# Optimization experiments

Hardware: AMD Instinct MI355X
Metric: run time of the kernel (lower is better)

## Reference

```python
import jax, jax.numpy as jnp
import numpy as np

B, C, L = 8, 256, 2048


def setup_inputs() -> dict:
    key = jax.random.key(0)
    ks = jax.random.split(key, 7)
    s = 0.05
    return {
        "x": jax.random.normal(ks[0], (B, C, L), dtype=jnp.float32),
        "Wq": jax.random.normal(ks[1], (C, C), dtype=jnp.float32) * s,
        "bq": jax.random.normal(ks[2], (C,), dtype=jnp.float32) * s,
        "Wk": jax.random.normal(ks[3], (C, C), dtype=jnp.float32) * s,
        "bk": jax.random.normal(ks[4], (C,), dtype=jnp.float32) * s,
        "Wv": jax.random.normal(ks[5], (C, C), dtype=jnp.float32) * s,
        "bv": jax.random.normal(ks[6], (C,), dtype=jnp.float32) * s,
    }


def reference(x, Wq, bq, Wk, bk, Wv, bv):
    # Conv1d with kernel_size=1 == per-position linear over channels.
    # x: [B, C, L]
    scale = x.shape[1] ** (-0.5)
    q = jnp.einsum('oc,bcl->bol', Wq, x) + bq[None, :, None]  # [B,C,L]
    k = jnp.einsum('oc,bcl->bol', Wk, x) + bk[None, :, None]
    v = jnp.einsum('oc,bcl->bol', Wv, x) + bv[None, :, None]
    scores = jnp.einsum('bcl,bcm->blm', q, k) * scale          # [B,L,L]
    attn = jax.nn.softmax(scores, axis=-1)
    context = jnp.einsum('blm,bcm->bcl', attn, v)              # [B,C,L]
    return context + x
```

## Files before the change

### kernel.cpp

```cpp
#include <hip/hip_runtime.h>

#define NB 8
#define NC 256
#define NL 2048
#define SCALE 0.0625f

typedef __attribute__((ext_vector_type(8))) __bf16 bf16x8;
typedef __attribute__((ext_vector_type(4))) float f32x4;
typedef __attribute__((ext_vector_type(4))) unsigned int u32x4;
typedef __attribute__((ext_vector_type(2))) unsigned int u32x2;
typedef __attribute__((ext_vector_type(4))) unsigned short u16x4;
typedef __attribute__((ext_vector_type(8))) unsigned short u16x8;

static __device__ __forceinline__ unsigned short f2b(float f) {
    unsigned int u = __builtin_bit_cast(unsigned int, f);
    u += 0x7fffu + ((u >> 16) & 1u);
    return (unsigned short)(u >> 16);
}

__global__ void wconv_kernel(const float* __restrict__ Wq,
                             const float* __restrict__ Wk,
                             const float* __restrict__ Wv,
                             unsigned short* __restrict__ Wbf)
{
    const int base = (blockIdx.x * 256 + threadIdx.x) * 4;
    const int mat  = base >> 16;
    const int off  = base & 65535;
    const float* W = (mat == 0) ? Wq : (mat == 1) ? Wk : Wv;
    float4 w = *(const float4*)&W[off];
    u16x4 p = {f2b(w.x), f2b(w.y), f2b(w.z), f2b(w.w)};
    *(u16x4*)&Wbf[base] = p;
}

__global__ __launch_bounds__(512, 4) void qkv_mfma(
    const float* __restrict__ x,
    const unsigned short* __restrict__ Wbf,
    const float* __restrict__ bq, const float* __restrict__ bk,
    const float* __restrict__ bv,
    unsigned short* __restrict__ qT, unsigned short* __restrict__ kT,
    unsigned short* __restrict__ vo)
{
    const int raw = blockIdx.x;
    const int b   = raw & 7;
    const int rem = raw >> 3;
    const int mat = rem >> 5;
    const int lt0 = (rem & 31) * 64;
    const int t    = threadIdx.x;
    const int w    = t >> 6;
    const int lane = t & 63;
    const int ln15 = lane & 15;
    const int quad = lane >> 4;

    __shared__ __align__(16) char qsmem[74240];
    unsigned short* XT = (unsigned short*)qsmem;
    unsigned short* WC = (unsigned short*)(qsmem + 32768);
    unsigned short (*Tr)[68] = (unsigned short(*)[68])(qsmem + 65536);
    unsigned short (*Vst)[68] = (unsigned short(*)[68])qsmem;

    const unsigned short* Wm = Wbf + mat * 65536;
    const float* bias = (mat == 0) ? bq : (mat == 1) ? bk : bv;

    float bvals[2][4];
    #pragma unroll
    for (int ot = 0; ot < 2; ++ot)
        #pragma unroll
        for (int r = 0; r < 4; ++r)
            bvals[ot][r] = bias[w * 32 + ot * 16 + quad * 4 + r];

    for (int cs = 0; cs < 4; ++cs) {
        const int c0 = cs * 64;
        #pragma unroll
        for (int p = 0; p < 2; ++p) {
            const int c  = p * 32 + (t >> 4);
            const int lg = t & 15;
            float4 xv = *(const float4*)&x[((size_t)(b * NC + c0 + c)) * NL + lt0 + lg * 4];
            u16x4 pk = {f2b(xv.x), f2b(xv.y), f2b(xv.z), f2b(xv.w)};
            *(u16x4*)&Tr[c][lg * 4] = pk;
        }
        __syncthreads();
        {
            const int l  = t >> 3;
            const int ck = t & 7;
            u16x8 o;
            #pragma unroll
            for (int i = 0; i < 8; ++i) o[i] = Tr[ck * 8 + i][l];
            const int g = (cs * 8 + ck) ^ (l & 15);
            *(u16x8*)&XT[l * 256 + g * 8] = o;
        }
        __syncthreads();
    }

    f32x4 acc[2][4];
    #pragma unroll
    for (int i = 0; i < 2; ++i)
        #pragma unroll
        for (int j = 0; j < 4; ++j) acc[i][j] = f32x4{0.f, 0.f, 0.f, 0.f};

    for (int k0 = 0; k0 < 4; ++k0) {
        if (k0) __syncthreads();
        #pragma unroll
        for (int s = 0; s < 4; ++s) {
            const int il = w * 4 + s;
            const int o  = il * 8 + (lane >> 3);
            const int p  = lane & 7;
            const int g  = p ^ (o & 7);
            const unsigned short* gp = &Wm[(size_t)o * NC + k0 * 64 + g * 8];
            __builtin_amdgcn_global_load_lds(
                (const __attribute__((address_space(1))) unsigned int*)gp,
                (__attribute__((address_space(3))) unsigned int*)&WC[il * 512],
                16, 0, 0);
        }
        __syncthreads();

        #pragma unroll
        for (int ks = 0; ks < 2; ++ks) {
            bf16x8 xf[4];
            #pragma unroll
            for (int lt = 0; lt < 4; ++lt) {
                const int l  = lt * 16 + ln15;
                const int kc = k0 * 8 + ks * 4 + quad;
                const int pp = kc ^ (l & 15);
                xf[lt] = __builtin_bit_cast(bf16x8, *(const u32x4*)&XT[l * 256 + pp * 8]);
            }
            #pragma unroll
            for (int ot = 0; ot < 2; ++ot) {
                const int o  = w * 32 + ot * 16 + ln15;
                const int pp = (ks * 4 + quad) ^ (o & 7);
                bf16x8 wf = __builtin_bit_cast(bf16x8, *(const u32x4*)&WC[o * 64 + pp * 8]);
                #pragma unroll
                for (int lt = 0; lt < 4; ++lt)
                    acc[ot][lt] = __builtin_amdgcn_mfma_f32_16x16x32_bf16(
                                      wf, xf[lt], acc[ot][lt], 0, 0, 0);
            }
        }
    }

    if (mat < 2) {
        unsigned short* out = (mat == 0) ? qT : kT;
        #pragma unroll
        for (int ot = 0; ot < 2; ++ot) {
            const int o_base = w * 32 + ot * 16 + quad * 4;
            #pragma unroll
            for (int lt = 0; lt < 4; ++lt) {
                const int l = lt0 + lt * 16 + ln15;
                u16x4 pk;
                #pragma unroll
                for (int r = 0; r < 4; ++r)
                    pk[r] = f2b(acc[ot][lt][r] + bvals[ot][r]);
                *(u16x4*)&out[((size_t)(b * NL + l)) * NC + o_base] = pk;
            }
        }
    } else {
        __syncthreads();
        #pragma unroll
        for (int ot = 0; ot < 2; ++ot)
            #pragma unroll
            for (int lt = 0; lt < 4; ++lt) {
                #pragma unroll
                for (int r = 0; r < 4; ++r) {
                    const int o = w * 32 + ot * 16 + quad * 4 + r;
                    Vst[o][lt * 16 + ln15] = f2b(acc[ot][lt][r] + bvals[ot][r]);
                }
            }
        __syncthreads();
        #pragma unroll
        for (int p = 0; p < 4; ++p) {
            const int row = (t >> 3) + 64 * p;
            const int col = (t & 7) * 8;
            u16x8 val = *(const u16x8*)&Vst[row][col];
            *(u16x8*)&vo[((size_t)(b * NC + row)) * NL + lt0 + col] = val;
        }
    }
}

__global__ __launch_bounds__(1024, 4) void attn_kernel(
    const unsigned short* __restrict__ qT,
    const unsigned short* __restrict__ kT,
    const unsigned short* __restrict__ v,
    const float* __restrict__ x,
    float* __restrict__ out)
{
    const int raw  = blockIdx.x;
    const int b    = raw & 7;
    const int l0   = (raw >> 3) * 64;
    const int t    = threadIdx.x;
    const int w    = t >> 6;
    const int lane = t & 63;
    const int ln15 = lane & 15;
    const int quad = lane >> 4;
    const int qg   = w & 3;
    const int kg   = w >> 2;

    __shared__ __align__(16) char smem[147456];
    unsigned short* Kb0 = (unsigned short*)smem;
    unsigned short* Vb0 = (unsigned short*)(smem + 32768);
    unsigned short* Kb1 = (unsigned short*)(smem + 65536);
    unsigned short* Vb1 = (unsigned short*)(smem + 98304);
    char* P0 = smem + 131072;
    char* P1 = smem + 139264;
    float (*buf)[68] = (float(*)[68])smem;

    bf16x8 qf[8];
    {
        const size_t qrow = ((size_t)b * NL + l0 + qg * 16 + ln15) * NC;
        #pragma unroll
        for (int kt = 0; kt < 8; ++kt)
            qf[kt] = __builtin_bit_cast(bf16x8,
                        *(const u32x4*)&qT[qrow + kt * 32 + quad * 8]);
    }

    f32x4 ctx[4];
    #pragma unroll
    for (int i = 0; i < 4; ++i) ctx[i] = f32x4{0.f, 0.f, 0.f, 0.f};
    f32x4 dacc = f32x4{0.f, 0.f, 0.f, 0.f};

    const u16x8 ones_u = {0x3F80, 0x3F80, 0x3F80, 0x3F80,
                          0x3F80, 0x3F80, 0x3F80, 0x3F80};
    const bf16x8 onesf = __builtin_bit_cast(bf16x8, ones_u);

    auto stageK = [&](int mt, unsigned short* Kd) {
        const int m0 = mt * 64;
        #pragma unroll
        for (int s = 0; s < 2; ++s) {
            const int il = w * 2 + s;
            const int n  = il * 2 + (lane >> 5);
            const int g  = (lane & 31) ^ (n & 15);
            const unsigned short* gp = &kT[((size_t)b * NL + m0 + n) * NC + g * 8];
            __builtin_amdgcn_global_load_lds(
                (const __attribute__((address_space(1))) unsigned int*)gp,
                (__attribute__((address_space(3))) unsigned int*)&Kd[il * 512],
                16, 0, 0);
        }
    };
    auto stageV = [&](int mt, unsigned short* Vd) {
        const int m0 = mt * 64;
        #pragma unroll
        for (int s = 0; s < 2; ++s) {
            const int il = w * 2 + s;
            const int c  = il * 8 + (lane >> 3);
            const int g  = (lane & 7) ^ (c & 7);
            const unsigned short* gp = &v[((size_t)(b * NC + c)) * NL + m0 + g * 8];
            __builtin_amdgcn_global_load_lds(
                (const __attribute__((address_space(1))) unsigned int*)gp,
                (__attribute__((address_space(3))) unsigned int*)&Vd[il * 512],
                16, 0, 0);
        }
    };

    const int q    = qg * 16 + ln15;
    const int pwof = q * 128 + (((kg * 32) + quad * 8) ^ ((q & 7) << 4));
    int prof[2];
    #pragma unroll
    for (int jw = 0; jw < 2; ++jw)
        prof[jw] = q * 128 + ((jw * 64 + quad * 16) ^ ((q & 7) << 4));

    stageK(0, Kb0);
    __syncthreads();

    for (int mt = 0; mt <= 32; ++mt) {
        if (mt < 31) stageK(mt + 1, (mt & 1) ? Kb0 : Kb1);
        if (mt < 32) stageV(mt, (mt & 1) ? Vb1 : Vb0);

        f32x4 sacc0 = f32x4{0.f, 0.f, 0.f, 0.f};
        f32x4 sacc1 = f32x4{0.f, 0.f, 0.f, 0.f};
        if (mt < 32) {
            const unsigned short* Kd = (mt & 1) ? Kb1 : Kb0;
            const int n = kg * 16 + ln15;
            #pragma unroll
            for (int kt = 0; kt < 8; kt += 2) {
                const int p0 = (kt * 4 + quad) ^ (n & 15);
                const int p1 = ((kt + 1) * 4 + quad) ^ (n & 15);
                bf16x8 kf0 = __builtin_bit_cast(bf16x8,
                               *(const u32x4*)&Kd[n * 256 + p0 * 8]);
                bf16x8 kf1 = __builtin_bit_cast(bf16x8,
                               *(const u32x4*)&Kd[n * 256 + p1 * 8]);
                sacc0 = __builtin_amdgcn_mfma_f32_16x16x32_bf16(
                            kf0, qf[kt], sacc0, 0, 0, 0);
                sacc1 = __builtin_amdgcn_mfma_f32_16x16x32_bf16(
                            kf1, qf[kt + 1], sacc1, 0, 0, 0);
            }
        }

        if (mt > 0) {
            const char* Pr = ((mt - 1) & 1) ? P1 : P0;
            const unsigned short* Vd = ((mt - 1) & 1) ? Vb1 : Vb0;
            bf16x8 pa[2];
            #pragma unroll
            for (int jw = 0; jw < 2; ++jw)
                pa[jw] = __builtin_bit_cast(bf16x8, *(const u32x4*)(Pr + prof[jw]));
            dacc = __builtin_amdgcn_mfma_f32_16x16x32_bf16(pa[0], onesf, dacc, 0, 0, 0);
            dacc = __builtin_amdgcn_mfma_f32_16x16x32_bf16(pa[1], onesf, dacc, 0, 0, 0);
            #pragma unroll
            for (int ct = 0; ct < 4; ++ct) {
                const int c = kg * 64 + ct * 16 + ln15;
                #pragma unroll
                for (int jw = 0; jw < 2; ++jw) {
                    const int p = (jw * 4 + quad) ^ (c & 7);
                    bf16x8 vb = __builtin_bit_cast(bf16x8,
                                  *(const u32x4*)&Vd[c * 64 + p * 8]);
                    ctx[ct] = __builtin_amdgcn_mfma_f32_16x16x32_bf16(
                                  pa[jw], vb, ctx[ct], 0, 0, 0);
                }
            }
        }

        if (mt < 32) {
            char* Pw = (mt & 1) ? P1 : P0;
            float e0 = __expf((sacc0[0] + sacc1[0]) * SCALE);
            float e1 = __expf((sacc0[1] + sacc1[1]) * SCALE);
            float e2 = __expf((sacc0[2] + sacc1[2]) * SCALE);
            float e3 = __expf((sacc0[3] + sacc1[3]) * SCALE);
            unsigned int d0 = (unsigned int)f2b(e0) | ((unsigned int)f2b(e1) << 16);
            unsigned int d1 = (unsigned int)f2b(e2) | ((unsigned int)f2b(e3) << 16);
            *(u32x2*)(Pw + pwof) = u32x2{d0, d1};
        }

        __syncthreads();
    }

    {
        float rinv[4];
        #pragma unroll
        for (int r = 0; r < 4; ++r) rinv[r] = 1.0f / dacc[r];
        #pragma unroll
        for (int ct = 0; ct < 4; ++ct) {
            const int c = kg * 64 + ct * 16 + ln15;
            #pragma unroll
            for (int r = 0; r < 4; ++r)
                buf[c][qg * 16 + quad * 4 + r] = ctx[ct][r] * rinv[r];
        }
    }
    __syncthreads();

    #pragma unroll
    for (int p = 0; p < 4; ++p) {
        const int f  = t + 1024 * p;
        const int c  = f >> 4;
        const int lg = (f & 15) * 4;
        const size_t idx = ((size_t)(b * NC + c)) * NL + l0 + lg;
        float4 xv = *(const float4*)&x[idx];
        float4 cv = *(const float4*)&buf[c][lg];
        float4 o = make_float4(cv.x + xv.x, cv.y + xv.y, cv.z + xv.z, cv.w + xv.w);
        *(float4*)&out[idx] = o;
    }
}

extern "C" void kernel_launch(void* const* d_in, const int* in_sizes, int n_in,
                              void* d_out, int out_size, void* d_ws, size_t ws_size,
                              hipStream_t stream) {
    const float* x  = (const float*)d_in[0];
    const float* Wq = (const float*)d_in[1];
    const float* bq = (const float*)d_in[2];
    const float* Wk = (const float*)d_in[3];
    const float* bk = (const float*)d_in[4];
    const float* Wv = (const float*)d_in[5];
    const float* bv = (const float*)d_in[6];
    float* out = (float*)d_out;

    const size_t plane = (size_t)NB * NC * NL;
    unsigned short* qT  = (unsigned short*)d_ws;
    unsigned short* kT  = qT + plane;
    unsigned short* v   = kT + plane;
    unsigned short* Wbf = v + plane;

    wconv_kernel<<<192, 256, 0, stream>>>(Wq, Wk, Wv, Wbf);

    qkv_mfma<<<768, 512, 0, stream>>>(x, Wbf, bq, bk, bv, qT, kT, v);

    attn_kernel<<<256, 1024, 0, stream>>>(qT, kT, v, x, out);
}
```

Baseline: 150.0 us.

## Load V fragments directly from global into registers and retile PV warps

Drops the LDS staging buffers for V and has each warp read its V fragments straight from global memory into registers. The P·V work is remapped so each warp owns 32 queries by 32 channels instead of 16 queries by 64 channels, which lets each V fragment be reused across two query rows. LDS use falls from 144KB to 80KB. In exchange, global load latency now sits on the PV critical path without async staging, and some V data is fetched redundantly by several warps through cache.

Result: slower. 192.4 us (+28.3%).

```diff
diff --git a/kernel.cpp b/kernel.cpp
--- a/kernel.cpp
+++ b/kernel.cpp
@@ -190,14 +190,14 @@
     const int quad = lane >> 4;
     const int qg   = w & 3;
     const int kg   = w >> 2;
-
-    __shared__ __align__(16) char smem[147456];
+    const int qh   = w >> 3;
+    const int ch   = w & 7;
+
+    __shared__ __align__(16) char smem[81920];
     unsigned short* Kb0 = (unsigned short*)smem;
-    unsigned short* Vb0 = (unsigned short*)(smem + 32768);
-    unsigned short* Kb1 = (unsigned short*)(smem + 65536);
-    unsigned short* Vb1 = (unsigned short*)(smem + 98304);
-    char* P0 = smem + 131072;
-    char* P1 = smem + 139264;
+    unsigned short* Kb1 = (unsigned short*)(smem + 32768);
+    char* P0 = smem + 65536;
+    char* P1 = smem + 73728;
     float (*buf)[68] = (float(*)[68])smem;
 
     bf16x8 qf[8];
@@ -209,10 +209,14 @@
                         *(const u32x4*)&qT[qrow + kt * 32 + quad * 8]);
     }
 
-    f32x4 ctx[4];
-    #pragma unroll
-    for (int i = 0; i < 4; ++i) ctx[i] = f32x4{0.f, 0.f, 0.f, 0.f};
-    f32x4 dacc = f32x4{0.f, 0.f, 0.f, 0.f};
+    f32x4 ctx[2][2];
+    #pragma unroll
+    for (int i = 0; i < 2; ++i)
+        #pragma unroll
+        for (int j = 0; j < 2; ++j) ctx[i][j] = f32x4{0.f, 0.f, 0.f, 0.f};
+    f32x4 dacc[2];
+    dacc[0] = f32x4{0.f, 0.f, 0.f, 0.f};
+    dacc[1] = f32x4{0.f, 0.f, 0.f, 0.f};
 
     const u16x8 ones_u = {0x3F80, 0x3F80, 0x3F80, 0x3F80,
                           0x3F80, 0x3F80, 0x3F80, 0x3F80};
@@ -232,34 +236,38 @@
                 16, 0, 0);
         }
     };
-    auto stageV = [&](int mt, unsigned short* Vd) {
-        const int m0 = mt * 64;
-        #pragma unroll
-        for (int s = 0; s < 2; ++s) {
-            const int il = w * 2 + s;
-            const int c  = il * 8 + (lane >> 3);
-            const int g  = (lane & 7) ^ (c & 7);
-            const unsigned short* gp = &v[((size_t)(b * NC + c)) * NL + m0 + g * 8];
-            __builtin_amdgcn_global_load_lds(
-                (const __attribute__((address_space(1))) unsigned int*)gp,
-                (__attribute__((address_space(3))) unsigned int*)&Vd[il * 512],
-                16, 0, 0);
-        }
-    };
 
     const int q    = qg * 16 + ln15;
     const int pwof = q * 128 + (((kg * 32) + quad * 8) ^ ((q & 7) << 4));
-    int prof[2];
-    #pragma unroll
-    for (int jw = 0; jw < 2; ++jw)
-        prof[jw] = q * 128 + ((jw * 64 + quad * 16) ^ ((q & 7) << 4));
+    int prof[2][2];
+    #pragma unroll
+    for (int row = 0; row < 2; ++row) {
+        const int qr = qh * 32 + row * 16 + ln15;
+        #pragma unroll
+        for (int jw = 0; jw < 2; ++jw)
+            prof[row][jw] = qr * 128 + ((jw * 64 + quad * 16) ^ ((qr & 7) << 4));
+    }
+    const unsigned short* vbase[2];
+    #pragma unroll
+    for (int ct = 0; ct < 2; ++ct)
+        vbase[ct] = v + ((size_t)(b * NC + ch * 32 + ct * 16 + ln15)) * NL + quad * 8;
 
     stageK(0, Kb0);
     __syncthreads();
 
     for (int mt = 0; mt <= 32; ++mt) {
         if (mt < 31) stageK(mt + 1, (mt & 1) ? Kb0 : Kb1);
-        if (mt < 32) stageV(mt, (mt & 1) ? Vb1 : Vb0);
+
+        bf16x8 vb[2][2];
+        if (mt > 0) {
+            const int m0 = (mt - 1) * 64;
+            #pragma unroll
+            for (int ct = 0; ct < 2; ++ct)
+                #pragma unroll
+                for (int jw = 0; jw < 2; ++jw)
+                    vb[ct][jw] = __builtin_bit_cast(bf16x8,
+                        *(const u32x4*)(vbase[ct] + m0 + jw * 32));
+        }
 
         f32x4 sacc0 = f32x4{0.f, 0.f, 0.f, 0.f};
         f32x4 sacc1 = f32x4{0.f, 0.f, 0.f, 0.f};
@@ -283,25 +291,29 @@
 
         if (mt > 0) {
             const char* Pr = ((mt - 1) & 1) ? P1 : P0;
-            const unsigned short* Vd = ((mt - 1) & 1) ? Vb1 : Vb0;
-            bf16x8 pa[2];
-            #pragma unroll
-            for (int jw = 0; jw < 2; ++jw)
-                pa[jw] = __builtin_bit_cast(bf16x8, *(const u32x4*)(Pr + prof[jw]));
-            dacc = __builtin_amdgcn_mfma_f32_16x16x32_bf16(pa[0], onesf, dacc, 0, 0, 0);
-            dacc = __builtin_amdgcn_mfma_f32_16x16x32_bf16(pa[1], onesf, dacc, 0, 0, 0);
-            #pragma unroll
-            for (int ct = 0; ct < 4; ++ct) {
-                const int c = kg * 64 + ct * 16 + ln15;
-                #pragma unroll
-                for (int jw = 0; jw < 2; ++jw) {
-                    const int p = (jw * 4 + quad) ^ (c & 7);
-                    bf16x8 vb = __builtin_bit_cast(bf16x8,
-                                  *(const u32x4*)&Vd[c * 64 + p * 8]);
-                    ctx[ct] = __builtin_amdgcn_mfma_f32_16x16x32_bf16(
-                                  pa[jw], vb, ctx[ct], 0, 0, 0);
+            bf16x8 pa[2][2];
+            #pragma unroll
+            for (int row = 0; row < 2; ++row)
+                #pragma unroll
+                for (int jw = 0; jw < 2; ++jw)
+                    pa[row][jw] = __builtin_bit_cast(bf16x8,
+                                     *(const u32x4*)(Pr + prof[row][jw]));
+            #pragma unroll
+            for (int row = 0; row < 2; ++row) {
+                dacc[row] = __builtin_amdgcn_mfma_f32_16x16x32_bf16(
+                                pa[row][0], onesf, dacc[row], 0, 0, 0);
+                dacc[row] = __builtin_amdgcn_mfma_f32_16x16x32_bf16(
+                                pa[row][1], onesf, dacc[row], 0, 0, 0);
+            }
+            #pragma unroll
+            for (int row = 0; row < 2; ++row)
+                #pragma unroll
+                for (int ct = 0; ct < 2; ++ct) {
+                    ctx[row][ct] = __builtin_amdgcn_mfma_f32_16x16x32_bf16(
+                                       pa[row][0], vb[ct][0], ctx[row][ct], 0, 0, 0);
+                    ctx[row][ct] = __builtin_amdgcn_mfma_f32_16x16x32_bf16(
+                                       pa[row][1], vb[ct][1], ctx[row][ct], 0, 0, 0);
                 }
-            }
         }
 
         if (mt < 32) {
@@ -319,15 +331,18 @@
     }
 
     {
-        float rinv[4];
-        #pragma unroll
-        for (int r = 0; r < 4; ++r) rinv[r] = 1.0f / dacc[r];
-        #pragma unroll
-        for (int ct = 0; ct < 4; ++ct) {
-            const int c = kg * 64 + ct * 16 + ln15;
-            #pragma unroll
-            for (int r = 0; r < 4; ++r)
-                buf[c][qg * 16 + quad * 4 + r] = ctx[ct][r] * rinv[r];
+        #pragma unroll
+        for (int row = 0; row < 2; ++row) {
+            float rinv[4];
+            #pragma unroll
+            for (int r = 0; r < 4; ++r) rinv[r] = 1.0f / dacc[row][r];
+            #pragma unroll
+            for (int ct = 0; ct < 2; ++ct) {
+                const int c = ch * 32 + ct * 16 + ln15;
+                #pragma unroll
+                for (int r = 0; r < 4; ++r)
+                    buf[c][qh * 32 + row * 16 + quad * 4 + r] = ctx[row][ct][r] * rinv[r];
+            }
         }
     }
     __syncthreads();
```
